# Optimization experiments

Measured on AMD Instinct MI355X. Metric: run time of the kernel, lower is better.

## Reference

```python
import jax, jax.numpy as jnp
import numpy as np

# Static problem constants (match setup_inputs)
K = 1024          # total objects across batch
B = 4             # number of row splits (events)
Q_MIN = 0.1
S_B = 1.0
BETA_EPS = 1e-3   # beta_scaling_epsilon
LSE_EPS = 1e-3    # continuous-max temperature in _beta_loss


def setup_inputs() -> dict:
    key = jax.random.key(0)
    k1, k2, k3, k4 = jax.random.split(key, 4)
    N = 100000
    C = 8
    K_per_B = K // B
    row_splits = jnp.array([0, 25000, 50000, 75000, 100000], dtype=jnp.int64)
    pt_rs = jnp.repeat(jnp.arange(B), N // B)  # row-split id per point
    # object ids local to each event, offset so objects are globally unique
    asso = jax.random.randint(k1, (N,), 0, K_per_B) + pt_rs * K_per_B
    noise = jax.random.uniform(k2, (N,)) < 0.10
    asso_idx = jnp.where(noise, -1, asso).astype(jnp.int64)
    beta = (jax.random.uniform(k3, (N, 1)) * 0.99 + 0.001).astype(jnp.float32)
    coords = jax.random.normal(k4, (N, C), dtype=jnp.float32)
    return {"beta": beta, "coords": coords, "asso_idx": asso_idx, "row_splits": row_splits}


def _oc_forward(beta, coords, asso_idx, row_splits):
    N = beta.shape[0]
    b = beta[:, 0]
    valid = asso_idx >= 0
    asso_c = jnp.where(valid, asso_idx, 0)
    fdt = coords.dtype

    # charge q = arctanh(clamped beta)^2 + q_min  (v_beta_scaling = arctanhsq)
    bc = jnp.clip(b, 0.0, 1.0 - BETA_EPS)
    q = jnp.arctanh(bc) ** 2 + Q_MIN

    # ---- alpha (condensation point) per object: argmax beta within object ----
    score = jnp.where(valid, b, -jnp.inf)
    seg_max = jax.ops.segment_max(score, asso_c, num_segments=K)
    is_alpha = valid & (score == seg_max[asso_c])
    alpha_idx = jax.ops.segment_max(jnp.where(is_alpha, jnp.arange(N), -1), asso_c, num_segments=K)
    N_k = jax.ops.segment_sum(valid.astype(fdt), asso_c, num_segments=K)
    obj_valid = N_k > 0
    a_idx = jnp.maximum(alpha_idx, 0)
    x_alpha = coords[a_idx]                                  # (K, C)
    q_alpha = jnp.where(obj_valid, q[a_idx], 0.0)            # (K,)

    # row-split id per point and per object
    pt_rs = jnp.searchsorted(row_splits, jnp.arange(N), side='right') - 1
    obj_rs = pt_rs[a_idx]

    # ---- attractive potential: each point pulled to its own alpha ----
    dsq_att = jnp.sum((coords - x_alpha[asso_c]) ** 2, axis=1)
    att = jnp.where(valid, q * q_alpha[asso_c] * dsq_att, 0.0)   # (N,)

    # ---- repulsive potential: every point vs every other object's alpha (same event) ----
    cn2 = jnp.sum(coords ** 2, axis=1)
    ck2 = jnp.sum(x_alpha ** 2, axis=1)
    dsq = jnp.maximum(cn2[:, None] + ck2[None, :] - 2.0 * (coords @ x_alpha.T), 0.0)  # (N, K)
    Vrep = jax.nn.relu(1.0 - jnp.sqrt(dsq + 1e-6))
    own = valid[:, None] & (asso_c[:, None] == jnp.arange(K)[None, :])
    mask = (obj_valid[None, :] & (pt_rs[:, None] == obj_rs[None, :]) & ~own).astype(fdt)
    # per-object repulsive norm: divide by N_k (fixed_repulsive_norm=None)
    rep = q * jnp.sum(Vrep * (q_alpha / jnp.maximum(N_k, 1.0))[None, :] * mask, axis=1)  # (N,)

    # ---- per-row-split means -> scalars ----
    lengths = (row_splits[1:] - row_splits[:-1]).astype(fdt)
    def rs_mean(x):
        return jax.ops.segment_sum(x, pt_rs, num_segments=B) / lengths
    L_V = jnp.mean(rs_mean(att))
    L_rep = jnp.mean(rs_mean(rep))

    # ---- beta loss: continuous max via logsumexp + short-circuit sum term ----
    m = jnp.where(obj_valid, seg_max, 0.0)
    lse_sum = jax.ops.segment_sum(jnp.where(valid, jnp.exp((b - m[asso_c]) / LSE_EPS), 0.0), asso_c, num_segments=K)
    lse = m + LSE_EPS * jnp.log(lse_sum + 1e-30)
    sum_b = jax.ops.segment_sum(jnp.where(valid, b, 0.0), asso_c, num_segments=K)
    beta_pen = (1.0 - lse) + (1.0 - jnp.clip(sum_b, 0.0, 1.0))   # (K,)
    obj_cnt = jax.ops.segment_sum(obj_valid.astype(fdt), obj_rs, num_segments=B)
    obj_pen_rs = jax.ops.segment_sum(jnp.where(obj_valid, beta_pen, 0.0), obj_rs, num_segments=B) / jnp.maximum(obj_cnt, 1.0)
    noise = ~valid
    noise_cnt = jax.ops.segment_sum(noise.astype(fdt), pt_rs, num_segments=B)
    noise_mean = jax.ops.segment_sum(jnp.where(noise, b, 0.0), pt_rs, num_segments=B) / jnp.maximum(noise_cnt, 1.0)
    L_b = jnp.mean(obj_pen_rs + S_B * noise_mean)

    # ---- payload scaling (p_beta_scaling = arctanhsq), normalized per object ----
    p = jnp.where(valid, jnp.maximum(jnp.arctanh(bc) ** 2, 1e-6), 0.0)
    p_sum = jax.ops.segment_sum(p, asso_c, num_segments=K)
    pl = jnp.where(valid, p / jnp.maximum(p_sum[asso_c], 1e-6), 0.0)
    pl = pl / jnp.maximum(obj_cnt[pt_rs], 1.0) / B   # normalize per object count and events

    L_V_rep = (att + rep)[:, None]
    return L_V, L_rep, L_b, pl[:, None], L_V_rep


def reference(beta, coords, asso_idx, row_splits):
    return _oc_forward(beta, coords, asso_idx, row_splits)
```

## Files before the change

kernel.cpp:

```cpp
#include <hip/hip_runtime.h>

#define NB1 64
#define B_RS 4

#define W_K    0
#define W_C    131072
#define W_SB   196608
#define W_SP   262144
#define W_NS   327680
#define A_CY0  328192
#define A_CY1  332288
#define A_LM   336384
#define A_EM   338432
#define A_SBM  342528
#define A_NKM  343552
#define A_OC   344576
#define A_LSE  344584
#define A_PP   352776

__device__ __forceinline__ unsigned fkey(float f) {
    unsigned u = __float_as_uint(f);
    return ((int)u < 0) ? ~u : (u | 0x80000000u);
}
__device__ __forceinline__ float fdec(unsigned k) {
    unsigned u = ((int)k < 0) ? (k & 0x7fffffffu) : ~k;
    return __uint_as_float(u);
}

__global__ __launch_bounds__(512) void k_p1(const float* __restrict__ beta,
                                            const int* __restrict__ asso,
                                            const int* __restrict__ rs,
                                            float* __restrict__ w, int N) {
    __shared__ unsigned long long sk[1024];
    __shared__ unsigned sc[1024];
    __shared__ float ssb[1024], ssp[1024];
    __shared__ float ns[8];
    int t = threadIdx.x, b = blockIdx.x;
    for (int j = t; j < 1024; j += 512) { sk[j] = 0ull; sc[j] = 0u; ssb[j] = 0.f; ssp[j] = 0.f; }
    if (t < 8) ns[t] = 0.f;
    int rs1 = rs[1], rs2 = rs[2], rs3 = rs[3];
    __syncthreads();
    for (int i = b * 512 + t; i < N; i += NB1 * 512) {
        float bv = beta[i];
        int a = asso[i];
        float bc = fminf(fmaxf(bv, 0.f), 0.999f);
        float ath = 0.5f * __logf(__fdividef(1.f + bc, 1.f - bc));
        float at2 = ath * ath;
        float pv = fmaxf(at2, 1e-6f);
        if (a >= 0) {
            unsigned long long pk = (((unsigned long long)fkey(bv)) << 32) | (unsigned)i;
            atomicMax(&sk[a], pk);
            atomicAdd(&sc[a], 1u);
            atomicAdd(&ssb[a], bv);
            atomicAdd(&ssp[a], pv);
        } else {
            int r = (i >= rs1) + (i >= rs2) + (i >= rs3);
            atomicAdd(&ns[2 * r], 1.f);
            atomicAdd(&ns[2 * r + 1], bv);
        }
    }
    __syncthreads();
    for (int j = t; j < 1024; j += 512) {
        ((unsigned long long*)w)[(b << 10) + j] = sk[j];
        ((unsigned*)w)[W_C + (b << 10) + j] = sc[j];
        w[W_SB + (b << 10) + j] = ssb[j];
        w[W_SP + (b << 10) + j] = ssp[j];
    }
    if (t < 8) w[W_NS + b * 8 + t] = ns[t];
}

__global__ __launch_bounds__(256) void k_m1(const float* __restrict__ beta,
                                            const float* __restrict__ coords,
                                            const int* __restrict__ rs,
                                            float* __restrict__ w) {
    __shared__ int oc0;
    int t = threadIdx.x, r = blockIdx.x;
    if (t == 0) oc0 = 0;
    int k = (r << 8) + t;
    unsigned long long k64 = 0ull;
    unsigned cnt = 0u;
    float sb = 0.f, sp = 0.f;
#pragma unroll 4
    for (int rp = 0; rp < NB1; ++rp) {
        unsigned long long v = ((const unsigned long long*)w)[(rp << 10) + k];
        k64 = v > k64 ? v : k64;
        cnt += ((const unsigned*)w)[W_C + (rp << 10) + k];
        sb += w[W_SB + (rp << 10) + k];
        sp += w[W_SP + (rp << 10) + k];
    }
    bool ov = cnt > 0u;
    int ai = (int)(unsigned)(k64 & 0xffffffffull);
    float4 x0 = ((const float4*)coords)[ai * 2];
    float4 x1 = ((const float4*)coords)[ai * 2 + 1];
    float ba = beta[ai];
    float bca = fminf(fmaxf(ba, 0.f), 0.999f);
    float ata = atanhf(bca);
    float qa = ov ? ata * ata + 0.1f : 0.f;
    float cf = qa / fmaxf((float)cnt, 1.f);
    ((float4*)(w + A_CY0))[k] = make_float4(-2.f * x0.x, -2.f * x0.y, -2.f * x0.z, -2.f * x0.w);
    ((float4*)(w + A_CY1))[k] = make_float4(-2.f * x1.x, -2.f * x1.y, -2.f * x1.z, -2.f * x1.w);
    float ck2 = x0.x * x0.x + x0.y * x0.y + x0.z * x0.z + x0.w * x0.w +
                x1.x * x1.x + x1.y * x1.y + x1.z * x1.z + x1.w * x1.w;
    ((float2*)(w + A_LM))[k] = make_float2(ck2 + 1e-6f, cf);
    ((float4*)(w + A_EM))[k] = make_float4(qa, sp, __uint_as_float((unsigned)(k64 >> 32)), 0.f);
    w[A_SBM + k] = sb;
    ((unsigned*)w)[A_NKM + k] = cnt;
    for (int j = t; j < 2048; j += 256) w[A_LSE + (r << 11) + j] = 0.f;
    __syncthreads();
    unsigned long long bal = __ballot(ov);
    if ((t & 63) == 0) atomicAdd(&oc0, __popcll(bal));
    __syncthreads();
    if (t == 0) w[A_OC + r] = (float)oc0;
}

__global__ __launch_bounds__(256) void k_p4(const float* __restrict__ beta,
                                            const float* __restrict__ coords,
                                            const int* __restrict__ asso,
                                            const int* __restrict__ rs,
                                            const float* __restrict__ wc,
                                            float* __restrict__ lse,
                                            float* __restrict__ pp,
                                            float* __restrict__ out, int N) {
    __shared__ float4 sY0[512];
    __shared__ float4 sY1[512];
    __shared__ float2 sLM[512];
    __shared__ float4 sEM[512];
    __shared__ float sOC[4];
    __shared__ float bins[8];
    int t = threadIdx.x, bid = blockIdx.x;
    int base = bid << 8;
    int rs1 = rs[1], rs2 = rs[2], rs3 = rs[3];
    int r0 = (base >= rs1) + (base >= rs2) + (base >= rs3);
    int lastp = min(base + 255, N - 1);
    int rl = (lastp >= rs1) + (lastp >= rs2) + (lastp >= rs3);
    {
        const float4* cy0 = (const float4*)(wc + A_CY0);
        const float4* cy1 = (const float4*)(wc + A_CY1);
        const float2* lm = (const float2*)(wc + A_LM);
        const float4* em = (const float4*)(wc + A_EM);
        int k0 = (r0 << 8) + t;
        sY0[t] = cy0[k0]; sY1[t] = cy1[k0]; sLM[t] = lm[k0]; sEM[t] = em[k0];
        if (rl != r0) {
            int k1 = (rl << 8) + t;
            sY0[256 + t] = cy0[k1]; sY1[256 + t] = cy1[k1];
            sLM[256 + t] = lm[k1]; sEM[256 + t] = em[k1];
        }
    }
    if (t < 4) sOC[t] = wc[A_OC + t];
    if (t < 8) bins[t] = 0.f;
    __syncthreads();
    int i = base + t;
    float att = 0.f, rep = 0.f;
    int r = r0;
    if (i < N) {
        const float4* cp = (const float4*)(coords + (size_t)i * 8);
        float4 c0 = cp[0], c1 = cp[1];
        float cn2 = c0.x * c0.x + c0.y * c0.y + c0.z * c0.z + c0.w * c0.w +
                    c1.x * c1.x + c1.y * c1.y + c1.z * c1.z + c1.w * c1.w;
        r = (i >= rs1) + (i >= rs2) + (i >= rs3);
        int s = (r == r0) ? 0 : 256;
        float acc = 0.f;
#pragma unroll 4
        for (int j = s; j < s + 256; ++j) {
            float4 y0 = sY0[j];
            float4 y1 = sY1[j];
            float2 cm = sLM[j];
            float d = cn2 + cm.x;
            d = fmaf(y0.x, c0.x, d); d = fmaf(y0.y, c0.y, d);
            d = fmaf(y0.z, c0.z, d); d = fmaf(y0.w, c0.w, d);
            d = fmaf(y1.x, c1.x, d); d = fmaf(y1.y, c1.y, d);
            d = fmaf(y1.z, c1.z, d); d = fmaf(y1.w, c1.w, d);
            d = fmaxf(d, 1e-6f);
            float v = fmaxf(1.f - sqrtf(d), 0.f);
            acc = fmaf(v, cm.y, acc);
        }
        float bv = beta[i];
        int aa = asso[i];
        float bc = fminf(fmaxf(bv, 0.f), 0.999f);
        float ath = 0.5f * __logf(__fdividef(1.f + bc, 1.f - bc));
        float at2 = ath * ath;
        float q = at2 + 0.1f;
        float pv = fmaxf(at2, 1e-6f);
        bool valid = aa >= 0;
        float pl = 0.f;
        if (valid) {
            int slot = (((aa >> 8) == r0) ? 0 : 256) + (aa & 255);
            float4 y0 = sY0[slot], y1 = sY1[slot];
            float2 cm = sLM[slot];
            float4 emv = sEM[slot];
            float d0 = c0.x + 0.5f * y0.x, d1 = c0.y + 0.5f * y0.y;
            float d2 = c0.z + 0.5f * y0.z, d3 = c0.w + 0.5f * y0.w;
            float d4 = c1.x + 0.5f * y1.x, d5 = c1.y + 0.5f * y1.y;
            float d6 = c1.z + 0.5f * y1.z, d7 = c1.w + 0.5f * y1.w;
            float dsq = d0 * d0 + d1 * d1 + d2 * d2 + d3 * d3 +
                        d4 * d4 + d5 * d5 + d6 * d6 + d7 * d7;
            att = q * emv.x * dsq;
            float d = cn2 + cm.x;
            d = fmaf(y0.x, c0.x, d); d = fmaf(y0.y, c0.y, d);
            d = fmaf(y0.z, c0.z, d); d = fmaf(y0.w, c0.w, d);
            d = fmaf(y1.x, c1.x, d); d = fmaf(y1.y, c1.y, d);
            d = fmaf(y1.z, c1.z, d); d = fmaf(y1.w, c1.w, d);
            d = fmaxf(d, 1e-6f);
            acc -= fmaxf(1.f - sqrtf(d), 0.f) * cm.y;
            float m = fdec(__float_as_uint(emv.z));
            atomicAdd(&lse[((bid & 7) << 10) + aa], __expf((bv - m) * 1000.f));
            pl = pv / fmaxf(emv.y, 1e-6f) / fmaxf(sOC[r], 1.f) * 0.25f;
        }
        rep = q * acc;
        out[3 + i] = pl;
        out[3 + N + i] = att + rep;
    }
    int lane = t & 63;
    int rA = __shfl(r, 0);
    bool uni = __all(r == rA);
    if (uni) {
        float aS = att, rS = rep;
#pragma unroll
        for (int o = 32; o; o >>= 1) { aS += __shfl_xor(aS, o); rS += __shfl_xor(rS, o); }
        if (lane == 0) { atomicAdd(&bins[rA], aS); atomicAdd(&bins[4 + rA], rS); }
    } else if (i < N) {
        atomicAdd(&bins[r], att);
        atomicAdd(&bins[4 + r], rep);
    }
    __syncthreads();
    if (t < 8) pp[bid * 8 + t] = bins[t];
}

__global__ __launch_bounds__(1024) void k_p5(const int* __restrict__ rs,
                                             const float* __restrict__ w,
                                             const float* __restrict__ pp, int nb,
                                             float* __restrict__ out) {
    __shared__ float op[4];
    __shared__ float nsb[8];
    __shared__ float ar8[8][9];
    int t = threadIdx.x;
    if (t < 4) op[t] = 0.f;
    __syncthreads();
    int k = t;
    float ls = 0.f;
#pragma unroll
    for (int rp = 0; rp < 8; ++rp) ls += w[A_LSE + (rp << 10) + k];
    unsigned cnt = ((const unsigned*)w)[A_NKM + k];
    bool ov = cnt > 0u;
    float4 emv = ((const float4*)(w + A_EM))[k];
    float m = ov ? fdec(__float_as_uint(emv.z)) : 0.f;
    float lsev = m + 0.001f * logf(ls + 1e-30f);
    float sbc = fminf(fmaxf(w[A_SBM + k], 0.f), 1.f);
    float bpen = ov ? (1.f - lsev) + (1.f - sbc) : 0.f;
    float v = bpen;
#pragma unroll
    for (int o = 32; o; o >>= 1) v += __shfl_xor(v, o);
    if ((t & 63) == 0) atomicAdd(&op[k >> 8], v);
    if (t < 64) {
        int slot = t & 7, part = t >> 3;
        float acc = 0.f;
        for (int j = part; j < nb; j += 8) acc += pp[j * 8 + slot];
        ar8[slot][part] = acc;
    } else if (t < 72) {
        int s = t - 64;
        float a = 0.f;
        for (int b = 0; b < NB1; ++b) a += w[W_NS + b * 8 + s];
        nsb[s] = a;
    }
    __syncthreads();
    if (t == 0) {
        float lv = 0.f, lr = 0.f, lb = 0.f;
        for (int r = 0; r < B_RS; ++r) {
            float a = 0.f, rp = 0.f;
            for (int j = 0; j < 8; ++j) { a += ar8[r][j]; rp += ar8[4 + r][j]; }
            float len = (float)(rs[r + 1] - rs[r]);
            lv += a / len;
            lr += rp / len;
            float oc = w[A_OC + r];
            lb += op[r] / fmaxf(oc, 1.f) + nsb[2 * r + 1] / fmaxf(nsb[2 * r], 1.f);
        }
        out[0] = lv * 0.25f;
        out[1] = lr * 0.25f;
        out[2] = lb * 0.25f;
    }
}

extern "C" void kernel_launch(void* const* d_in, const int* in_sizes, int n_in,
                              void* d_out, int out_size, void* d_ws, size_t ws_size,
                              hipStream_t stream) {
    const float* beta = (const float*)d_in[0];
    const float* coords = (const float*)d_in[1];
    const int* asso = (const int*)d_in[2];
    const int* rs = (const int*)d_in[3];
    int N = in_sizes[0];
    float* w = (float*)d_ws;
    float* out = (float*)d_out;
    int nb = (N + 255) / 256;
    hipLaunchKernelGGL(k_p1, dim3(NB1), dim3(512), 0, stream, beta, asso, rs, w, N);
    hipLaunchKernelGGL(k_m1, dim3(4), dim3(256), 0, stream, beta, coords, rs, w);
    hipLaunchKernelGGL(k_p4, dim3(nb), dim3(256), 0, stream, beta, coords, asso, rs,
                       w, w + A_LSE, w + A_PP, out, N);
    hipLaunchKernelGGL(k_p5, dim3(1), dim3(1024), 0, stream, rs, w, w + A_PP, nb, out);
}
```

Measured before the change: 65.10 us.

## Split repulsion over object chunks, two points per thread, fuse final reduction

The main pairwise kernel now splits each 256-point tile's 256 objects into four 64-object chunks handled by separate 128-thread blocks. Each thread processes two points, reusing every shared-memory object load for both. Per-point outputs are accumulated with global atomics into a buffer that the first kernel zeroes. The separate final reduction kernel is removed and replaced by a last-block-done ticket pattern inside the main kernel. This aims to raise parallelism and cut a launch, at the cost of extra global atomics, duplicated coordinate loads per chunk, and a serialized tail in the last block.

```diff
diff --git a/kernel.cpp b/kernel.cpp
--- a/kernel.cpp
+++ b/kernel.cpp
@@ -16,7 +16,8 @@
 #define A_NKM  343552
 #define A_OC   344576
 #define A_LSE  344584
-#define A_PP   352776
+#define A_BIN  352776
+#define A_TK   353288
 
 __device__ __forceinline__ unsigned fkey(float f) {
     unsigned u = __float_as_uint(f);
@@ -30,7 +31,8 @@
 __global__ __launch_bounds__(512) void k_p1(const float* __restrict__ beta,
                                             const int* __restrict__ asso,
                                             const int* __restrict__ rs,
-                                            float* __restrict__ w, int N) {
+                                            float* __restrict__ w,
+                                            float* __restrict__ out, int N) {
     __shared__ unsigned long long sk[1024];
     __shared__ unsigned sc[1024];
     __shared__ float ssb[1024], ssp[1024];
@@ -43,6 +45,7 @@
     for (int i = b * 512 + t; i < N; i += NB1 * 512) {
         float bv = beta[i];
         int a = asso[i];
+        out[3 + N + i] = 0.f;
         float bc = fminf(fmaxf(bv, 0.f), 0.999f);
         float ath = 0.5f * __logf(__fdividef(1.f + bc, 1.f - bc));
         float at2 = ath * ath;
@@ -102,10 +105,14 @@
     float ck2 = x0.x * x0.x + x0.y * x0.y + x0.z * x0.z + x0.w * x0.w +
                 x1.x * x1.x + x1.y * x1.y + x1.z * x1.z + x1.w * x1.w;
     ((float2*)(w + A_LM))[k] = make_float2(ck2 + 1e-6f, cf);
-    ((float4*)(w + A_EM))[k] = make_float4(qa, sp, __uint_as_float((unsigned)(k64 >> 32)), 0.f);
+    ((float4*)(w + A_EM))[k] = make_float4(qa, sp, __uint_as_float((unsigned)(k64 >> 32)), cf);
     w[A_SBM + k] = sb;
     ((unsigned*)w)[A_NKM + k] = cnt;
     for (int j = t; j < 2048; j += 256) w[A_LSE + (r << 11) + j] = 0.f;
+    if (r == 0) {
+        for (int j = t; j < 512; j += 256) w[A_BIN + j] = 0.f;
+        if (t == 0) ((unsigned*)w)[A_TK] = 0u;
+    }
     __syncthreads();
     unsigned long long bal = __ballot(ov);
     if ((t & 63) == 0) atomicAdd(&oc0, __popcll(bal));
@@ -113,170 +120,225 @@
     if (t == 0) w[A_OC + r] = (float)oc0;
 }
 
-__global__ __launch_bounds__(256) void k_p4(const float* __restrict__ beta,
+__global__ __launch_bounds__(128) void k_p4(const float* __restrict__ beta,
                                             const float* __restrict__ coords,
                                             const int* __restrict__ asso,
                                             const int* __restrict__ rs,
                                             const float* __restrict__ wc,
                                             float* __restrict__ lse,
-                                            float* __restrict__ pp,
+                                            float* __restrict__ bin,
+                                            unsigned* __restrict__ tk,
                                             float* __restrict__ out, int N) {
-    __shared__ float4 sY0[512];
-    __shared__ float4 sY1[512];
-    __shared__ float2 sLM[512];
-    __shared__ float4 sEM[512];
-    __shared__ float sOC[4];
+    __shared__ float4 sY0[128], sY1[128];
+    __shared__ float2 sLM[128];
     __shared__ float bins[8];
+    __shared__ int sLast;
     int t = threadIdx.x, bid = blockIdx.x;
-    int base = bid << 8;
+    int pc = bid >> 2, cc = bid & 3;
+    int base = pc << 8;
     int rs1 = rs[1], rs2 = rs[2], rs3 = rs[3];
     int r0 = (base >= rs1) + (base >= rs2) + (base >= rs3);
     int lastp = min(base + 255, N - 1);
     int rl = (lastp >= rs1) + (lastp >= rs2) + (lastp >= rs3);
+    const float4* cy0 = (const float4*)(wc + A_CY0);
+    const float4* cy1 = (const float4*)(wc + A_CY1);
+    const float2* lmt = (const float2*)(wc + A_LM);
+    if (t < 64) {
+        int k0 = (r0 << 8) + (cc << 6) + t;
+        sY0[t] = cy0[k0]; sY1[t] = cy1[k0]; sLM[t] = lmt[k0];
+    } else if (rl != r0) {
+        int j = t - 64;
+        int k1 = (rl << 8) + (cc << 6) + j;
+        sY0[t] = cy0[k1]; sY1[t] = cy1[k1]; sLM[t] = lmt[k1];
+    }
+    if (t < 8) bins[t] = 0.f;
+    __syncthreads();
+    int i0 = base + 2 * t, i1 = i0 + 1;
+    bool in0 = i0 < N, in1 = i1 < N;
+    float att0 = 0.f, att1 = 0.f, rep0 = 0.f, rep1 = 0.f;
+    int rr0 = r0, rr1 = r0;
+    if (in0) {
+        const float4* cp = (const float4*)(coords + (size_t)i0 * 8);
+        float4 c00 = cp[0], c01 = cp[1], c10, c11;
+        float cn20 = c00.x * c00.x + c00.y * c00.y + c00.z * c00.z + c00.w * c00.w +
+                     c01.x * c01.x + c01.y * c01.y + c01.z * c01.z + c01.w * c01.w;
+        float cn21 = 0.f;
+        rr0 = (i0 >= rs1) + (i0 >= rs2) + (i0 >= rs3);
+        if (in1) {
+            c10 = cp[2]; c11 = cp[3];
+            cn21 = c10.x * c10.x + c10.y * c10.y + c10.z * c10.z + c10.w * c10.w +
+                   c11.x * c11.x + c11.y * c11.y + c11.z * c11.z + c11.w * c11.w;
+            rr1 = (i1 >= rs1) + (i1 >= rs2) + (i1 >= rs3);
+        }
+        int s0 = (rr0 == r0) ? 0 : 64;
+        int s1 = (rr1 == r0) ? 0 : 64;
+        float acc0 = 0.f, acc1 = 0.f;
+        if (in1 && s0 == s1) {
+#pragma unroll 2
+            for (int j = s0; j < s0 + 64; ++j) {
+                float4 y0 = sY0[j];
+                float4 y1 = sY1[j];
+                float2 cm = sLM[j];
+                float d0 = cn20 + cm.x, d1 = cn21 + cm.x;
+                d0 = fmaf(y0.x, c00.x, d0); d1 = fmaf(y0.x, c10.x, d1);
+                d0 = fmaf(y0.y, c00.y, d0); d1 = fmaf(y0.y, c10.y, d1);
+                d0 = fmaf(y0.z, c00.z, d0); d1 = fmaf(y0.z, c10.z, d1);
+                d0 = fmaf(y0.w, c00.w, d0); d1 = fmaf(y0.w, c10.w, d1);
+                d0 = fmaf(y1.x, c01.x, d0); d1 = fmaf(y1.x, c11.x, d1);
+                d0 = fmaf(y1.y, c01.y, d0); d1 = fmaf(y1.y, c11.y, d1);
+                d0 = fmaf(y1.z, c01.z, d0); d1 = fmaf(y1.z, c11.z, d1);
+                d0 = fmaf(y1.w, c01.w, d0); d1 = fmaf(y1.w, c11.w, d1);
+                d0 = fmaxf(d0, 1e-6f); d1 = fmaxf(d1, 1e-6f);
+                float v0 = fmaxf(1.f - sqrtf(d0), 0.f);
+                float v1 = fmaxf(1.f - sqrtf(d1), 0.f);
+                acc0 = fmaf(v0, cm.y, acc0);
+                acc1 = fmaf(v1, cm.y, acc1);
+            }
+        } else {
+#pragma unroll 2
+            for (int j = s0; j < s0 + 64; ++j) {
+                float4 y0 = sY0[j]; float4 y1 = sY1[j]; float2 cm = sLM[j];
+                float d = cn20 + cm.x;
+                d = fmaf(y0.x, c00.x, d); d = fmaf(y0.y, c00.y, d);
+                d = fmaf(y0.z, c00.z, d); d = fmaf(y0.w, c00.w, d);
+                d = fmaf(y1.x, c01.x, d); d = fmaf(y1.y, c01.y, d);
+                d = fmaf(y1.z, c01.z, d); d = fmaf(y1.w, c01.w, d);
+                d = fmaxf(d, 1e-6f);
+                acc0 = fmaf(fmaxf(1.f - sqrtf(d), 0.f), cm.y, acc0);
+            }
+            if (in1) {
+#pragma unroll 2
+                for (int j = s1; j < s1 + 64; ++j) {
+                    float4 y0 = sY0[j]; float4 y1 = sY1[j]; float2 cm = sLM[j];
+                    float d = cn21 + cm.x;
+                    d = fmaf(y0.x, c10.x, d); d = fmaf(y0.y, c10.y, d);
+                    d = fmaf(y0.z, c10.z, d); d = fmaf(y0.w, c10.w, d);
+                    d = fmaf(y1.x, c11.x, d); d = fmaf(y1.y, c11.y, d);
+                    d = fmaf(y1.z, c11.z, d); d = fmaf(y1.w, c11.w, d);
+                    d = fmaxf(d, 1e-6f);
+                    acc1 = fmaf(fmaxf(1.f - sqrtf(d), 0.f), cm.y, acc1);
+                }
+            }
+        }
+        float2 b2; int2 a2;
+        if (in1) { b2 = *(const float2*)(beta + i0); a2 = *(const int2*)(asso + i0); }
+        else { b2.x = beta[i0]; b2.y = 0.f; a2.x = asso[i0]; a2.y = -1; }
+#pragma unroll
+        for (int p = 0; p < 2; ++p) {
+            if (p && !in1) break;
+            int i = p ? i1 : i0;
+            float bv = p ? b2.y : b2.x;
+            int aa = p ? a2.y : a2.x;
+            float acc = p ? acc1 : acc0;
+            float4 cA = p ? c10 : c00;
+            float4 cB = p ? c11 : c01;
+            float cn2 = p ? cn21 : cn20;
+            int r = p ? rr1 : rr0;
+            float bc = fminf(fmaxf(bv, 0.f), 0.999f);
+            float ath = 0.5f * __logf(__fdividef(1.f + bc, 1.f - bc));
+            float at2 = ath * ath;
+            float q = at2 + 0.1f;
+            if (cc == 0) {
+                float attv = 0.f, pl = 0.f;
+                if (aa >= 0) {
+                    float4 y0 = cy0[aa], y1 = cy1[aa];
+                    float4 em = ((const float4*)(wc + A_EM))[aa];
+                    float d0 = cA.x + 0.5f * y0.x, d1 = cA.y + 0.5f * y0.y;
+                    float d2 = cA.z + 0.5f * y0.z, d3 = cA.w + 0.5f * y0.w;
+                    float d4 = cB.x + 0.5f * y1.x, d5 = cB.y + 0.5f * y1.y;
+                    float d6 = cB.z + 0.5f * y1.z, d7 = cB.w + 0.5f * y1.w;
+                    float dsq = d0 * d0 + d1 * d1 + d2 * d2 + d3 * d3 +
+                                d4 * d4 + d5 * d5 + d6 * d6 + d7 * d7;
+                    attv = q * em.x * dsq;
+                    float yy = y0.x * y0.x + y0.y * y0.y + y0.z * y0.z + y0.w * y0.w +
+                               y1.x * y1.x + y1.y * y1.y + y1.z * y1.z + y1.w * y1.w;
+                    float d = cn2 + fmaf(0.25f, yy, 1e-6f);
+                    d = fmaf(y0.x, cA.x, d); d = fmaf(y0.y, cA.y, d);
+                    d = fmaf(y0.z, cA.z, d); d = fmaf(y0.w, cA.w, d);
+                    d = fmaf(y1.x, cB.x, d); d = fmaf(y1.y, cB.y, d);
+                    d = fmaf(y1.z, cB.z, d); d = fmaf(y1.w, cB.w, d);
+                    d = fmaxf(d, 1e-6f);
+                    acc -= fmaxf(1.f - sqrtf(d), 0.f) * em.w;
+                    float m = fdec(__float_as_uint(em.z));
+                    atomicAdd(&lse[((bid & 7) << 10) + aa], __expf((bv - m) * 1000.f));
+                    float pv = fmaxf(at2, 1e-6f);
+                    pl = pv / fmaxf(em.y, 1e-6f) / fmaxf(wc[A_OC + r], 1.f) * 0.25f;
+                }
+                float repc = q * acc;
+                out[3 + i] = pl;
+                atomicAdd(&out[3 + N + i], attv + repc);
+                if (p) { att1 = attv; rep1 = repc; } else { att0 = attv; rep0 = repc; }
+            } else {
+                float repc = q * acc;
+                atomicAdd(&out[3 + N + i], repc);
+                if (p) rep1 = repc; else rep0 = repc;
+            }
+        }
+    }
     {
-        const float4* cy0 = (const float4*)(wc + A_CY0);
-        const float4* cy1 = (const float4*)(wc + A_CY1);
-        const float2* lm = (const float2*)(wc + A_LM);
-        const float4* em = (const float4*)(wc + A_EM);
-        int k0 = (r0 << 8) + t;
-        sY0[t] = cy0[k0]; sY1[t] = cy1[k0]; sLM[t] = lm[k0]; sEM[t] = em[k0];
-        if (rl != r0) {
-            int k1 = (rl << 8) + t;
-            sY0[256 + t] = cy0[k1]; sY1[256 + t] = cy1[k1];
-            sLM[256 + t] = lm[k1]; sEM[256 + t] = em[k1];
-        }
-    }
-    if (t < 4) sOC[t] = wc[A_OC + t];
-    if (t < 8) bins[t] = 0.f;
-    __syncthreads();
-    int i = base + t;
-    float att = 0.f, rep = 0.f;
-    int r = r0;
-    if (i < N) {
-        const float4* cp = (const float4*)(coords + (size_t)i * 8);
-        float4 c0 = cp[0], c1 = cp[1];
-        float cn2 = c0.x * c0.x + c0.y * c0.y + c0.z * c0.z + c0.w * c0.w +
-                    c1.x * c1.x + c1.y * c1.y + c1.z * c1.z + c1.w * c1.w;
-        r = (i >= rs1) + (i >= rs2) + (i >= rs3);
-        int s = (r == r0) ? 0 : 256;
-        float acc = 0.f;
-#pragma unroll 4
-        for (int j = s; j < s + 256; ++j) {
-            float4 y0 = sY0[j];
-            float4 y1 = sY1[j];
-            float2 cm = sLM[j];
-            float d = cn2 + cm.x;
-            d = fmaf(y0.x, c0.x, d); d = fmaf(y0.y, c0.y, d);
-            d = fmaf(y0.z, c0.z, d); d = fmaf(y0.w, c0.w, d);
-            d = fmaf(y1.x, c1.x, d); d = fmaf(y1.y, c1.y, d);
-            d = fmaf(y1.z, c1.z, d); d = fmaf(y1.w, c1.w, d);
-            d = fmaxf(d, 1e-6f);
-            float v = fmaxf(1.f - sqrtf(d), 0.f);
-            acc = fmaf(v, cm.y, acc);
-        }
-        float bv = beta[i];
-        int aa = asso[i];
-        float bc = fminf(fmaxf(bv, 0.f), 0.999f);
-        float ath = 0.5f * __logf(__fdividef(1.f + bc, 1.f - bc));
-        float at2 = ath * ath;
-        float q = at2 + 0.1f;
-        float pv = fmaxf(at2, 1e-6f);
-        bool valid = aa >= 0;
-        float pl = 0.f;
-        if (valid) {
-            int slot = (((aa >> 8) == r0) ? 0 : 256) + (aa & 255);
-            float4 y0 = sY0[slot], y1 = sY1[slot];
-            float2 cm = sLM[slot];
-            float4 emv = sEM[slot];
-            float d0 = c0.x + 0.5f * y0.x, d1 = c0.y + 0.5f * y0.y;
-            float d2 = c0.z + 0.5f * y0.z, d3 = c0.w + 0.5f * y0.w;
-            float d4 = c1.x + 0.5f * y1.x, d5 = c1.y + 0.5f * y1.y;
-            float d6 = c1.z + 0.5f * y1.z, d7 = c1.w + 0.5f * y1.w;
-            float dsq = d0 * d0 + d1 * d1 + d2 * d2 + d3 * d3 +
-                        d4 * d4 + d5 * d5 + d6 * d6 + d7 * d7;
-            att = q * emv.x * dsq;
-            float d = cn2 + cm.x;
-            d = fmaf(y0.x, c0.x, d); d = fmaf(y0.y, c0.y, d);
-            d = fmaf(y0.z, c0.z, d); d = fmaf(y0.w, c0.w, d);
-            d = fmaf(y1.x, c1.x, d); d = fmaf(y1.y, c1.y, d);
-            d = fmaf(y1.z, c1.z, d); d = fmaf(y1.w, c1.w, d);
-            d = fmaxf(d, 1e-6f);
-            acc -= fmaxf(1.f - sqrtf(d), 0.f) * cm.y;
-            float m = fdec(__float_as_uint(emv.z));
-            atomicAdd(&lse[((bid & 7) << 10) + aa], __expf((bv - m) * 1000.f));
-            pl = pv / fmaxf(emv.y, 1e-6f) / fmaxf(sOC[r], 1.f) * 0.25f;
-        }
-        rep = q * acc;
-        out[3 + i] = pl;
-        out[3 + N + i] = att + rep;
-    }
-    int lane = t & 63;
-    int rA = __shfl(r, 0);
-    bool uni = __all(r == rA);
-    if (uni) {
-        float aS = att, rS = rep;
+        int rA = __shfl(rr0, 0);
+        bool uni = __all(rr0 == rA) && __all(rr1 == rA);
+        int lane = t & 63;
+        if (uni) {
+            float aS = att0 + att1, rS = rep0 + rep1;
 #pragma unroll
-        for (int o = 32; o; o >>= 1) { aS += __shfl_xor(aS, o); rS += __shfl_xor(rS, o); }
-        if (lane == 0) { atomicAdd(&bins[rA], aS); atomicAdd(&bins[4 + rA], rS); }
-    } else if (i < N) {
-        atomicAdd(&bins[r], att);
-        atomicAdd(&bins[4 + r], rep);
-    }
-    __syncthreads();
-    if (t < 8) pp[bid * 8 + t] = bins[t];
-}
-
-__global__ __launch_bounds__(1024) void k_p5(const int* __restrict__ rs,
-                                             const float* __restrict__ w,
-                                             const float* __restrict__ pp, int nb,
-                                             float* __restrict__ out) {
-    __shared__ float op[4];
-    __shared__ float nsb[8];
-    __shared__ float ar8[8][9];
-    int t = threadIdx.x;
-    if (t < 4) op[t] = 0.f;
-    __syncthreads();
-    int k = t;
-    float ls = 0.f;
+            for (int o = 32; o; o >>= 1) { aS += __shfl_xor(aS, o); rS += __shfl_xor(rS, o); }
+            if (lane == 0) { atomicAdd(&bins[rA], aS); atomicAdd(&bins[4 + rA], rS); }
+        } else {
+            if (in0) { atomicAdd(&bins[rr0], att0); atomicAdd(&bins[4 + rr0], rep0); }
+            if (in1) { atomicAdd(&bins[rr1], att1); atomicAdd(&bins[4 + rr1], rep1); }
+        }
+    }
+    __syncthreads();
+    if (t < 8) atomicAdd(&bin[(bid & 63) * 8 + t], bins[t]);
+    if (t == 0) {
+        __threadfence();
+        unsigned tkv = atomicAdd(tk, 1u);
+        sLast = (tkv == gridDim.x - 1) ? 1 : 0;
+    }
+    __syncthreads();
+    if (sLast) {
+        __threadfence();
+        __shared__ float sOP[4], sAR[8], sNS[8];
+        if (t < 4) sOP[t] = 0.f;
+        __syncthreads();
+        if (t < 8) {
+            float a = 0.f;
+            for (int j = 0; j < 64; ++j) a += bin[j * 8 + t];
+            sAR[t] = a;
+        } else if (t < 16) {
+            int s = t - 8;
+            float a = 0.f;
+            for (int b = 0; b < NB1; ++b) a += wc[W_NS + b * 8 + s];
+            sNS[s] = a;
+        }
+        for (int k = t; k < 1024; k += 128) {
+            unsigned cnt = ((const unsigned*)wc)[A_NKM + k];
+            if (cnt > 0u) {
+                float ls = 0.f;
 #pragma unroll
-    for (int rp = 0; rp < 8; ++rp) ls += w[A_LSE + (rp << 10) + k];
-    unsigned cnt = ((const unsigned*)w)[A_NKM + k];
-    bool ov = cnt > 0u;
-    float4 emv = ((const float4*)(w + A_EM))[k];
-    float m = ov ? fdec(__float_as_uint(emv.z)) : 0.f;
-    float lsev = m + 0.001f * logf(ls + 1e-30f);
-    float sbc = fminf(fmaxf(w[A_SBM + k], 0.f), 1.f);
-    float bpen = ov ? (1.f - lsev) + (1.f - sbc) : 0.f;
-    float v = bpen;
-#pragma unroll
-    for (int o = 32; o; o >>= 1) v += __shfl_xor(v, o);
-    if ((t & 63) == 0) atomicAdd(&op[k >> 8], v);
-    if (t < 64) {
-        int slot = t & 7, part = t >> 3;
-        float acc = 0.f;
-        for (int j = part; j < nb; j += 8) acc += pp[j * 8 + slot];
-        ar8[slot][part] = acc;
-    } else if (t < 72) {
-        int s = t - 64;
-        float a = 0.f;
-        for (int b = 0; b < NB1; ++b) a += w[W_NS + b * 8 + s];
-        nsb[s] = a;
-    }
-    __syncthreads();
-    if (t == 0) {
-        float lv = 0.f, lr = 0.f, lb = 0.f;
-        for (int r = 0; r < B_RS; ++r) {
-            float a = 0.f, rp = 0.f;
-            for (int j = 0; j < 8; ++j) { a += ar8[r][j]; rp += ar8[4 + r][j]; }
-            float len = (float)(rs[r + 1] - rs[r]);
-            lv += a / len;
-            lr += rp / len;
-            float oc = w[A_OC + r];
-            lb += op[r] / fmaxf(oc, 1.f) + nsb[2 * r + 1] / fmaxf(nsb[2 * r], 1.f);
-        }
-        out[0] = lv * 0.25f;
-        out[1] = lr * 0.25f;
-        out[2] = lb * 0.25f;
+                for (int rp = 0; rp < 8; ++rp) ls += lse[(rp << 10) + k];
+                float4 em = ((const float4*)(wc + A_EM))[k];
+                float m = fdec(__float_as_uint(em.z));
+                float lsev = m + 0.001f * logf(ls + 1e-30f);
+                float sbc = fminf(fmaxf(wc[A_SBM + k], 0.f), 1.f);
+                atomicAdd(&sOP[k >> 8], (1.f - lsev) + (1.f - sbc));
+            }
+        }
+        __syncthreads();
+        if (t == 0) {
+            float lv = 0.f, lr = 0.f, lb = 0.f;
+            for (int r = 0; r < B_RS; ++r) {
+                float len = (float)(rs[r + 1] - rs[r]);
+                lv += sAR[r] / len;
+                lr += sAR[4 + r] / len;
+                float oc = wc[A_OC + r];
+                lb += sOP[r] / fmaxf(oc, 1.f) + sNS[2 * r + 1] / fmaxf(sNS[2 * r], 1.f);
+            }
+            out[0] = lv * 0.25f;
+            out[1] = lr * 0.25f;
+            out[2] = lb * 0.25f;
+        }
     }
 }
 
@@ -290,10 +352,9 @@
     int N = in_sizes[0];
     float* w = (float*)d_ws;
     float* out = (float*)d_out;
-    int nb = (N + 255) / 256;
-    hipLaunchKernelGGL(k_p1, dim3(NB1), dim3(512), 0, stream, beta, asso, rs, w, N);
+    int npc = (N + 255) / 256;
+    hipLaunchKernelGGL(k_p1, dim3(NB1), dim3(512), 0, stream, beta, asso, rs, w, out, N);
     hipLaunchKernelGGL(k_m1, dim3(4), dim3(256), 0, stream, beta, coords, rs, w);
-    hipLaunchKernelGGL(k_p4, dim3(nb), dim3(256), 0, stream, beta, coords, asso, rs,
-                       w, w + A_LSE, w + A_PP, out, N);
-    hipLaunchKernelGGL(k_p5, dim3(1), dim3(1024), 0, stream, rs, w, w + A_PP, nb, out);
-}
+    hipLaunchKernelGGL(k_p4, dim3(npc * 4), dim3(128), 0, stream, beta, coords, asso, rs,
+                       w, w + A_LSE, w + A_BIN, (unsigned*)(w + A_TK), out, N);
+}
```

After: 110.2 us. 1.69x slower.

## Split repulsion loop across two threads, fuse final reduce via last-block ticket

Applied to the files above, without the earlier changes.

k_m1 now uses four threads per object to reduce the 64 partial slices, combining them with shuffles. In k_p4 each point's 256-object repulsion loop is split across two threads, whose halves meet in shared memory. The final reduction kernel k_p5 is folded into k_p4's last block through an atomic ticket counter with threadfences, and hardware sqrt replaces sqrtf. The aim is more parallelism and one fewer launch. The cost is extra global atomics on the bin arrays and the attraction-side loads moving from LDS to global memory.

```diff
diff --git a/kernel.cpp b/kernel.cpp
--- a/kernel.cpp
+++ b/kernel.cpp
@@ -16,7 +16,8 @@
 #define A_NKM  343552
 #define A_OC   344576
 #define A_LSE  344584
-#define A_PP   352776
+#define A_BIN  352776
+#define A_TK   353288
 
 __device__ __forceinline__ unsigned fkey(float f) {
     unsigned u = __float_as_uint(f);
@@ -26,6 +27,7 @@
     unsigned u = ((int)k < 0) ? (k & 0x7fffffffu) : ~k;
     return __uint_as_float(u);
 }
+__device__ __forceinline__ float fsq(float x) { return __builtin_amdgcn_sqrtf(x); }
 
 __global__ __launch_bounds__(512) void k_p1(const float* __restrict__ beta,
                                             const int* __restrict__ asso,
@@ -69,99 +71,117 @@
     if (t < 8) w[W_NS + b * 8 + t] = ns[t];
 }
 
-__global__ __launch_bounds__(256) void k_m1(const float* __restrict__ beta,
-                                            const float* __restrict__ coords,
-                                            const int* __restrict__ rs,
-                                            float* __restrict__ w) {
+__global__ __launch_bounds__(1024) void k_m1(const float* __restrict__ beta,
+                                             const float* __restrict__ coords,
+                                             const int* __restrict__ rs,
+                                             float* __restrict__ w) {
     __shared__ int oc0;
     int t = threadIdx.x, r = blockIdx.x;
     if (t == 0) oc0 = 0;
-    int k = (r << 8) + t;
+    int ci = t >> 2, sub = t & 3;
+    int k = (r << 8) + ci;
     unsigned long long k64 = 0ull;
     unsigned cnt = 0u;
     float sb = 0.f, sp = 0.f;
 #pragma unroll 4
-    for (int rp = 0; rp < NB1; ++rp) {
+    for (int m = 0; m < 16; ++m) {
+        int rp = sub * 16 + m;
         unsigned long long v = ((const unsigned long long*)w)[(rp << 10) + k];
         k64 = v > k64 ? v : k64;
         cnt += ((const unsigned*)w)[W_C + (rp << 10) + k];
         sb += w[W_SB + (rp << 10) + k];
         sp += w[W_SP + (rp << 10) + k];
     }
+    {
+        unsigned long long o = __shfl_xor(k64, 1); k64 = o > k64 ? o : k64;
+        o = __shfl_xor(k64, 2); k64 = o > k64 ? o : k64;
+        cnt += __shfl_xor(cnt, 1); cnt += __shfl_xor(cnt, 2);
+        sb += __shfl_xor(sb, 1); sb += __shfl_xor(sb, 2);
+        sp += __shfl_xor(sp, 1); sp += __shfl_xor(sp, 2);
+    }
     bool ov = cnt > 0u;
-    int ai = (int)(unsigned)(k64 & 0xffffffffull);
-    float4 x0 = ((const float4*)coords)[ai * 2];
-    float4 x1 = ((const float4*)coords)[ai * 2 + 1];
-    float ba = beta[ai];
-    float bca = fminf(fmaxf(ba, 0.f), 0.999f);
-    float ata = atanhf(bca);
-    float qa = ov ? ata * ata + 0.1f : 0.f;
-    float cf = qa / fmaxf((float)cnt, 1.f);
-    ((float4*)(w + A_CY0))[k] = make_float4(-2.f * x0.x, -2.f * x0.y, -2.f * x0.z, -2.f * x0.w);
-    ((float4*)(w + A_CY1))[k] = make_float4(-2.f * x1.x, -2.f * x1.y, -2.f * x1.z, -2.f * x1.w);
-    float ck2 = x0.x * x0.x + x0.y * x0.y + x0.z * x0.z + x0.w * x0.w +
-                x1.x * x1.x + x1.y * x1.y + x1.z * x1.z + x1.w * x1.w;
-    ((float2*)(w + A_LM))[k] = make_float2(ck2 + 1e-6f, cf);
-    ((float4*)(w + A_EM))[k] = make_float4(qa, sp, __uint_as_float((unsigned)(k64 >> 32)), 0.f);
-    w[A_SBM + k] = sb;
-    ((unsigned*)w)[A_NKM + k] = cnt;
-    for (int j = t; j < 2048; j += 256) w[A_LSE + (r << 11) + j] = 0.f;
-    __syncthreads();
-    unsigned long long bal = __ballot(ov);
+    if (sub == 0) {
+        int ai = (int)(unsigned)(k64 & 0xffffffffull);
+        float4 x0 = ((const float4*)coords)[ai * 2];
+        float4 x1 = ((const float4*)coords)[ai * 2 + 1];
+        float ba = beta[ai];
+        float bca = fminf(fmaxf(ba, 0.f), 0.999f);
+        float ata = atanhf(bca);
+        float qa = ov ? ata * ata + 0.1f : 0.f;
+        float cf = qa / fmaxf((float)cnt, 1.f);
+        ((float4*)(w + A_CY0))[k] = make_float4(-2.f * x0.x, -2.f * x0.y, -2.f * x0.z, -2.f * x0.w);
+        ((float4*)(w + A_CY1))[k] = make_float4(-2.f * x1.x, -2.f * x1.y, -2.f * x1.z, -2.f * x1.w);
+        float ck2 = x0.x * x0.x + x0.y * x0.y + x0.z * x0.z + x0.w * x0.w +
+                    x1.x * x1.x + x1.y * x1.y + x1.z * x1.z + x1.w * x1.w;
+        ((float2*)(w + A_LM))[k] = make_float2(ck2 + 1e-6f, cf);
+        ((float4*)(w + A_EM))[k] = make_float4(qa, sp, __uint_as_float((unsigned)(k64 >> 32)), cf);
+        w[A_SBM + k] = sb;
+        ((unsigned*)w)[A_NKM + k] = cnt;
+    }
+    for (int j = t; j < 2048; j += 1024) w[A_LSE + (r << 11) + j] = 0.f;
+    if (r == 0) {
+        if (t < 512) w[A_BIN + t] = 0.f;
+        if (t == 0) ((unsigned*)w)[A_TK] = 0u;
+    }
+    __syncthreads();
+    unsigned long long bal = __ballot(ov && sub == 0);
     if ((t & 63) == 0) atomicAdd(&oc0, __popcll(bal));
     __syncthreads();
     if (t == 0) w[A_OC + r] = (float)oc0;
 }
 
-__global__ __launch_bounds__(256) void k_p4(const float* __restrict__ beta,
+__global__ __launch_bounds__(512) void k_p4(const float* __restrict__ beta,
                                             const float* __restrict__ coords,
                                             const int* __restrict__ asso,
                                             const int* __restrict__ rs,
                                             const float* __restrict__ wc,
                                             float* __restrict__ lse,
-                                            float* __restrict__ pp,
+                                            float* __restrict__ bin,
+                                            unsigned* __restrict__ tk,
                                             float* __restrict__ out, int N) {
-    __shared__ float4 sY0[512];
-    __shared__ float4 sY1[512];
+    __shared__ float4 sY0[512], sY1[512];
     __shared__ float2 sLM[512];
-    __shared__ float4 sEM[512];
+    __shared__ float sAcc[512];
     __shared__ float sOC[4];
     __shared__ float bins[8];
+    __shared__ int sLast;
     int t = threadIdx.x, bid = blockIdx.x;
     int base = bid << 8;
     int rs1 = rs[1], rs2 = rs[2], rs3 = rs[3];
     int r0 = (base >= rs1) + (base >= rs2) + (base >= rs3);
     int lastp = min(base + 255, N - 1);
     int rl = (lastp >= rs1) + (lastp >= rs2) + (lastp >= rs3);
-    {
-        const float4* cy0 = (const float4*)(wc + A_CY0);
-        const float4* cy1 = (const float4*)(wc + A_CY1);
-        const float2* lm = (const float2*)(wc + A_LM);
-        const float4* em = (const float4*)(wc + A_EM);
+    const float4* cy0 = (const float4*)(wc + A_CY0);
+    const float4* cy1 = (const float4*)(wc + A_CY1);
+    const float2* lmt = (const float2*)(wc + A_LM);
+    const float4* emt = (const float4*)(wc + A_EM);
+    if (t < 256) {
         int k0 = (r0 << 8) + t;
-        sY0[t] = cy0[k0]; sY1[t] = cy1[k0]; sLM[t] = lm[k0]; sEM[t] = em[k0];
-        if (rl != r0) {
-            int k1 = (rl << 8) + t;
-            sY0[256 + t] = cy0[k1]; sY1[256 + t] = cy1[k1];
-            sLM[256 + t] = lm[k1]; sEM[256 + t] = em[k1];
-        }
+        sY0[t] = cy0[k0]; sY1[t] = cy1[k0]; sLM[t] = lmt[k0];
+    } else if (rl != r0) {
+        int k1 = (rl << 8) + (t - 256);
+        sY0[t] = cy0[k1]; sY1[t] = cy1[k1]; sLM[t] = lmt[k1];
     }
     if (t < 4) sOC[t] = wc[A_OC + t];
     if (t < 8) bins[t] = 0.f;
     __syncthreads();
-    int i = base + t;
-    float att = 0.f, rep = 0.f;
+    int pi = t & 255, half = t >> 8;
+    int i = base + pi;
+    bool in = i < N;
+    float acc = 0.f;
     int r = r0;
-    if (i < N) {
+    float4 c0, c1;
+    float cn2 = 0.f;
+    if (in) {
         const float4* cp = (const float4*)(coords + (size_t)i * 8);
-        float4 c0 = cp[0], c1 = cp[1];
-        float cn2 = c0.x * c0.x + c0.y * c0.y + c0.z * c0.z + c0.w * c0.w +
-                    c1.x * c1.x + c1.y * c1.y + c1.z * c1.z + c1.w * c1.w;
+        c0 = cp[0]; c1 = cp[1];
+        cn2 = c0.x * c0.x + c0.y * c0.y + c0.z * c0.z + c0.w * c0.w +
+              c1.x * c1.x + c1.y * c1.y + c1.z * c1.z + c1.w * c1.w;
         r = (i >= rs1) + (i >= rs2) + (i >= rs3);
         int s = (r == r0) ? 0 : 256;
-        float acc = 0.f;
+        int js = s + half * 128, je = js + 128;
 #pragma unroll 4
-        for (int j = s; j < s + 256; ++j) {
+        for (int j = js; j < je; ++j) {
             float4 y0 = sY0[j];
             float4 y1 = sY1[j];
             float2 cm = sLM[j];
@@ -171,112 +191,115 @@
             d = fmaf(y1.x, c1.x, d); d = fmaf(y1.y, c1.y, d);
             d = fmaf(y1.z, c1.z, d); d = fmaf(y1.w, c1.w, d);
             d = fmaxf(d, 1e-6f);
-            float v = fmaxf(1.f - sqrtf(d), 0.f);
+            float v = fmaxf(1.f - fsq(d), 0.f);
             acc = fmaf(v, cm.y, acc);
         }
+    }
+    sAcc[t] = acc;
+    __syncthreads();
+    float att = 0.f, rep = 0.f;
+    if (t < 256 && in) {
+        float total = sAcc[t] + sAcc[t + 256];
         float bv = beta[i];
         int aa = asso[i];
         float bc = fminf(fmaxf(bv, 0.f), 0.999f);
         float ath = 0.5f * __logf(__fdividef(1.f + bc, 1.f - bc));
         float at2 = ath * ath;
         float q = at2 + 0.1f;
-        float pv = fmaxf(at2, 1e-6f);
-        bool valid = aa >= 0;
         float pl = 0.f;
-        if (valid) {
-            int slot = (((aa >> 8) == r0) ? 0 : 256) + (aa & 255);
-            float4 y0 = sY0[slot], y1 = sY1[slot];
-            float2 cm = sLM[slot];
-            float4 emv = sEM[slot];
+        if (aa >= 0) {
+            float4 y0 = cy0[aa], y1 = cy1[aa];
+            float2 cm = lmt[aa];
+            float4 em = emt[aa];
             float d0 = c0.x + 0.5f * y0.x, d1 = c0.y + 0.5f * y0.y;
             float d2 = c0.z + 0.5f * y0.z, d3 = c0.w + 0.5f * y0.w;
             float d4 = c1.x + 0.5f * y1.x, d5 = c1.y + 0.5f * y1.y;
             float d6 = c1.z + 0.5f * y1.z, d7 = c1.w + 0.5f * y1.w;
             float dsq = d0 * d0 + d1 * d1 + d2 * d2 + d3 * d3 +
                         d4 * d4 + d5 * d5 + d6 * d6 + d7 * d7;
-            att = q * emv.x * dsq;
+            att = q * em.x * dsq;
             float d = cn2 + cm.x;
             d = fmaf(y0.x, c0.x, d); d = fmaf(y0.y, c0.y, d);
             d = fmaf(y0.z, c0.z, d); d = fmaf(y0.w, c0.w, d);
             d = fmaf(y1.x, c1.x, d); d = fmaf(y1.y, c1.y, d);
             d = fmaf(y1.z, c1.z, d); d = fmaf(y1.w, c1.w, d);
             d = fmaxf(d, 1e-6f);
-            acc -= fmaxf(1.f - sqrtf(d), 0.f) * cm.y;
-            float m = fdec(__float_as_uint(emv.z));
+            total -= fmaxf(1.f - fsq(d), 0.f) * cm.y;
+            float m = fdec(__float_as_uint(em.z));
             atomicAdd(&lse[((bid & 7) << 10) + aa], __expf((bv - m) * 1000.f));
-            pl = pv / fmaxf(emv.y, 1e-6f) / fmaxf(sOC[r], 1.f) * 0.25f;
-        }
-        rep = q * acc;
+            float pv = fmaxf(at2, 1e-6f);
+            pl = pv / fmaxf(em.y, 1e-6f) / fmaxf(sOC[r], 1.f) * 0.25f;
+        }
+        rep = q * total;
         out[3 + i] = pl;
         out[3 + N + i] = att + rep;
     }
-    int lane = t & 63;
-    int rA = __shfl(r, 0);
-    bool uni = __all(r == rA);
-    if (uni) {
-        float aS = att, rS = rep;
+    if (t < 256) {
+        int rA = __shfl(r, 0);
+        bool uni = __all(r == rA);
+        int lane = t & 63;
+        if (uni) {
+            float aS = att, rS = rep;
 #pragma unroll
-        for (int o = 32; o; o >>= 1) { aS += __shfl_xor(aS, o); rS += __shfl_xor(rS, o); }
-        if (lane == 0) { atomicAdd(&bins[rA], aS); atomicAdd(&bins[4 + rA], rS); }
-    } else if (i < N) {
-        atomicAdd(&bins[r], att);
-        atomicAdd(&bins[4 + r], rep);
-    }
-    __syncthreads();
-    if (t < 8) pp[bid * 8 + t] = bins[t];
-}
-
-__global__ __launch_bounds__(1024) void k_p5(const int* __restrict__ rs,
-                                             const float* __restrict__ w,
-                                             const float* __restrict__ pp, int nb,
-                                             float* __restrict__ out) {
-    __shared__ float op[4];
-    __shared__ float nsb[8];
-    __shared__ float ar8[8][9];
-    int t = threadIdx.x;
-    if (t < 4) op[t] = 0.f;
-    __syncthreads();
-    int k = t;
-    float ls = 0.f;
+            for (int o = 32; o; o >>= 1) { aS += __shfl_xor(aS, o); rS += __shfl_xor(rS, o); }
+            if (lane == 0) { atomicAdd(&bins[rA], aS); atomicAdd(&bins[4 + rA], rS); }
+        } else if (in) {
+            atomicAdd(&bins[r], att);
+            atomicAdd(&bins[4 + r], rep);
+        }
+    }
+    __syncthreads();
+    if (t < 8) atomicAdd(&bin[(bid & 63) * 8 + t], bins[t]);
+    if (t == 0) {
+        __threadfence();
+        unsigned tkv = atomicAdd(tk, 1u);
+        sLast = (tkv == gridDim.x - 1) ? 1 : 0;
+    }
+    __syncthreads();
+    if (sLast) {
+        __threadfence();
+        __shared__ float sOP[4], sAR[8], sNS[8];
+        if (t < 4) sOP[t] = 0.f;
+        __syncthreads();
+        if (t < 64) {
+            int s = t & 7, g = t >> 3;
+            float a = 0.f, n = 0.f;
 #pragma unroll
-    for (int rp = 0; rp < 8; ++rp) ls += w[A_LSE + (rp << 10) + k];
-    unsigned cnt = ((const unsigned*)w)[A_NKM + k];
-    bool ov = cnt > 0u;
-    float4 emv = ((const float4*)(w + A_EM))[k];
-    float m = ov ? fdec(__float_as_uint(emv.z)) : 0.f;
-    float lsev = m + 0.001f * logf(ls + 1e-30f);
-    float sbc = fminf(fmaxf(w[A_SBM + k], 0.f), 1.f);
-    float bpen = ov ? (1.f - lsev) + (1.f - sbc) : 0.f;
-    float v = bpen;
+            for (int m = 0; m < 8; ++m) {
+                a += bin[(g + 8 * m) * 8 + s];
+                n += wc[W_NS + (g + 8 * m) * 8 + s];
+            }
+            a += __shfl_xor(a, 8); a += __shfl_xor(a, 16); a += __shfl_xor(a, 32);
+            n += __shfl_xor(n, 8); n += __shfl_xor(n, 16); n += __shfl_xor(n, 32);
+            if (t < 8) { sAR[t] = a; sNS[t] = n; }
+        }
+        for (int k = t; k < 1024; k += 512) {
+            unsigned cnt = ((const unsigned*)wc)[A_NKM + k];
+            if (cnt > 0u) {
+                float ls = 0.f;
 #pragma unroll
-    for (int o = 32; o; o >>= 1) v += __shfl_xor(v, o);
-    if ((t & 63) == 0) atomicAdd(&op[k >> 8], v);
-    if (t < 64) {
-        int slot = t & 7, part = t >> 3;
-        float acc = 0.f;
-        for (int j = part; j < nb; j += 8) acc += pp[j * 8 + slot];
-        ar8[slot][part] = acc;
-    } else if (t < 72) {
-        int s = t - 64;
-        float a = 0.f;
-        for (int b = 0; b < NB1; ++b) a += w[W_NS + b * 8 + s];
-        nsb[s] = a;
-    }
-    __syncthreads();
-    if (t == 0) {
-        float lv = 0.f, lr = 0.f, lb = 0.f;
-        for (int r = 0; r < B_RS; ++r) {
-            float a = 0.f, rp = 0.f;
-            for (int j = 0; j < 8; ++j) { a += ar8[r][j]; rp += ar8[4 + r][j]; }
-            float len = (float)(rs[r + 1] - rs[r]);
-            lv += a / len;
-            lr += rp / len;
-            float oc = w[A_OC + r];
-            lb += op[r] / fmaxf(oc, 1.f) + nsb[2 * r + 1] / fmaxf(nsb[2 * r], 1.f);
-        }
-        out[0] = lv * 0.25f;
-        out[1] = lr * 0.25f;
-        out[2] = lb * 0.25f;
+                for (int rp = 0; rp < 8; ++rp) ls += lse[(rp << 10) + k];
+                float4 em = ((const float4*)(wc + A_EM))[k];
+                float m = fdec(__float_as_uint(em.z));
+                float lsev = m + 0.001f * logf(ls + 1e-30f);
+                float sbc = fminf(fmaxf(wc[A_SBM + k], 0.f), 1.f);
+                atomicAdd(&sOP[k >> 8], (1.f - lsev) + (1.f - sbc));
+            }
+        }
+        __syncthreads();
+        if (t == 0) {
+            float lv = 0.f, lr = 0.f, lb = 0.f;
+            for (int r2 = 0; r2 < B_RS; ++r2) {
+                float len = (float)(rs[r2 + 1] - rs[r2]);
+                lv += sAR[r2] / len;
+                lr += sAR[4 + r2] / len;
+                float oc = wc[A_OC + r2];
+                lb += sOP[r2] / fmaxf(oc, 1.f) + sNS[2 * r2 + 1] / fmaxf(sNS[2 * r2], 1.f);
+            }
+            out[0] = lv * 0.25f;
+            out[1] = lr * 0.25f;
+            out[2] = lb * 0.25f;
+        }
     }
 }
 
@@ -292,8 +315,7 @@
     float* out = (float*)d_out;
     int nb = (N + 255) / 256;
     hipLaunchKernelGGL(k_p1, dim3(NB1), dim3(512), 0, stream, beta, asso, rs, w, N);
-    hipLaunchKernelGGL(k_m1, dim3(4), dim3(256), 0, stream, beta, coords, rs, w);
-    hipLaunchKernelGGL(k_p4, dim3(nb), dim3(256), 0, stream, beta, coords, asso, rs,
-                       w, w + A_LSE, w + A_PP, out, N);
-    hipLaunchKernelGGL(k_p5, dim3(1), dim3(1024), 0, stream, rs, w, w + A_PP, nb, out);
-}
+    hipLaunchKernelGGL(k_m1, dim3(4), dim3(1024), 0, stream, beta, coords, rs, w);
+    hipLaunchKernelGGL(k_p4, dim3(nb), dim3(512), 0, stream, beta, coords, asso, rs,
+                       w, w + A_LSE, w + A_BIN, (unsigned*)(w + A_TK), out, N);
+}
```

Result: faster. 54.70 us, median of 2 (-16.0%).
